# Kernel tuning notes

Measured on AMD Instinct MI355X. Metric: run time of the kernel, lower is better.

## Reference

```python
import jax, jax.numpy as jnp
import numpy as np

B, T, E, H = 4, 2048, 1024, 16
D = E // H
PAD_TOKEN_ID = 0
VOCAB = 50257


def setup_inputs() -> dict:
    key = jax.random.key(0)
    k1, k2, k3, k4 = jax.random.split(key, 4)
    x = jax.random.normal(k1, (B, T, E), dtype=jnp.float32)
    input_ids = jax.random.randint(k2, (B, T), 0, VOCAB, dtype=jnp.int64)
    # guarantee first key of every sequence is non-pad so no softmax row is fully masked
    input_ids = input_ids.at[:, 0].set(1)
    w_qkv = jax.random.normal(k3, (E, 3 * E), dtype=jnp.float32) * 0.02
    w_out = jax.random.normal(k4, (E, E), dtype=jnp.float32) * 0.02
    b_out = jnp.zeros((E,), dtype=jnp.float32)
    return {"x": x, "input_ids": input_ids, "w_qkv": w_qkv, "w_out": w_out, "b_out": b_out}


def reference(x, input_ids, w_qkv, w_out, b_out):
    b, t, e = x.shape
    # fused QKV projection (bias=False in original)
    qkv = x @ w_qkv                                   # [B,T,3E]
    q, k, v = jnp.split(qkv, 3, axis=-1)
    q = q.reshape(b, t, H, D).transpose(0, 2, 1, 3)   # [B,H,T,D]
    k = k.reshape(b, t, H, D).transpose(0, 2, 1, 3)
    v = v.reshape(b, t, H, D).transpose(0, 2, 1, 3)

    scale = 1.0 / jnp.sqrt(jnp.asarray(D, dtype=x.dtype))
    scores = jnp.einsum("bhqd,bhkd->bhqk", q, k) * scale   # [B,H,T,T]

    causal = jnp.tril(jnp.ones((t, t), dtype=bool))         # [T,T]
    key_keep = (input_ids != PAD_TOKEN_ID)[:, None, None, :]  # [B,1,1,T]
    mask = causal[None, None, :, :] & key_keep               # [B,1(T broadcast over H),T,T]
    scores = jnp.where(mask, scores, -jnp.inf)

    attn = jax.nn.softmax(scores, axis=-1)                   # dropout_p=0 in eval
    y = jnp.einsum("bhqk,bhkd->bhqd", attn, v)               # [B,H,T,D]
    y = y.transpose(0, 2, 1, 3).reshape(b, t, e)             # [B,T,E]
    return y @ w_out + b_out
```

## Files before the change

kernel.cpp:

```cpp
#include <hip/hip_runtime.h>
#include <hip/hip_bf16.h>
#include <stdint.h>

#define Hn 16
#define Tn 2048
#define En 1024
#define Dh 64

typedef __bf16 bf16x8 __attribute__((ext_vector_type(8)));
typedef float f32x4 __attribute__((ext_vector_type(4)));
typedef unsigned short u16;
typedef u16 u16x8 __attribute__((ext_vector_type(8)));

#define SCALE_Q 0.18033688f

__device__ __forceinline__ u16 f2bf(float f) {
  union { float f; uint32_t u; } v; v.f = f;
  uint32_t r = v.u + 0x7fffu + ((v.u >> 16) & 1u);
  return (u16)(r >> 16);
}

typedef const __attribute__((address_space(1))) void gvoid_t;
typedef __attribute__((address_space(3))) void lvoid_t;
__device__ __forceinline__ void gl_lds16(const void* g, void* l) {
  __builtin_amdgcn_global_load_lds((gvoid_t*)g, (lvoid_t*)l, 16, 0, 0);
}

__global__ void cvt_x_k(const float* __restrict__ in, u16* __restrict__ out) {
  int i = (blockIdx.x * 256 + threadIdx.x) * 8;
  float4 a = *(const float4*)(in + i);
  float4 b = *(const float4*)(in + i + 4);
  u16x8 o;
  o[0] = f2bf(a.x); o[1] = f2bf(a.y); o[2] = f2bf(a.z); o[3] = f2bf(a.w);
  o[4] = f2bf(b.x); o[5] = f2bf(b.y); o[6] = f2bf(b.z); o[7] = f2bf(b.w);
  *(u16x8*)(out + i) = o;
}

__global__ void transpose_cvt_k(const float* __restrict__ in, u16* __restrict__ out,
                                int R, int C) {
  __shared__ float tile[32][33];
  int c0 = blockIdx.x * 32, r0 = blockIdx.y * 32;
  for (int i = threadIdx.y; i < 32; i += 8)
    tile[i][threadIdx.x] = in[(size_t)(r0 + i) * C + c0 + threadIdx.x];
  __syncthreads();
  for (int i = threadIdx.y; i < 32; i += 8)
    out[(size_t)(c0 + i) * R + r0 + threadIdx.x] = f2bf(tile[threadIdx.x][i]);
}

__global__ void prep_mask_k(const int* __restrict__ in, float* __restrict__ maskf) {
  __shared__ int is64_s;
  if (threadIdx.x == 0) {
    int all0 = 1;
    for (int i = 1; i < 256; i += 2) all0 &= (in[i] == 0);
    is64_s = all0;
  }
  __syncthreads();
  int i = blockIdx.x * 256 + threadIdx.x;
  int v = is64_s ? in[2 * i] : in[i];
  maskf[i] = (v != 0) ? 0.f : -1e30f;
}

__device__ __forceinline__ void gemm_mainloop(const u16* __restrict__ A,
                                              const u16* __restrict__ Bt,
                                              int K, int m0, int n0,
                                              u16* lds, f32x4 acc[4][4]) {
  const int tid = threadIdx.x;
  const int lane = tid & 63;
  const int w = tid >> 6;
  const int wm = (w >> 1) * 64, wn = (w & 1) * 64;
  const int quad = lane >> 4, ln = lane & 15;

  const int e0 = w * 512 + lane * 8;
  const int r0 = e0 >> 5, c0 = e0 & 31;

  const u16* gA0 = A + (size_t)(m0 + r0) * K + c0;
  const u16* gA1 = gA0 + (size_t)64 * K;
  const u16* gB0 = Bt + (size_t)(n0 + r0) * K + c0;
  const u16* gB1 = gB0 + (size_t)64 * K;
  u16* lA0 = lds + e0;
  u16* lA1 = lds + e0 + 2048;
  u16* lB0 = lds + e0 + 4096;
  u16* lB1 = lds + e0 + 6144;

  for (int k0 = 0; k0 < K; k0 += 32) {
    gl_lds16(gA0 + k0, lA0);
    gl_lds16(gA1 + k0, lA1);
    gl_lds16(gB0 + k0, lB0);
    gl_lds16(gB1 + k0, lB1);
    __syncthreads();
    bf16x8 af[4], bfr[4];
#pragma unroll
    for (int mt = 0; mt < 4; mt++)
      af[mt] = *(const bf16x8*)(lds + (wm + mt * 16 + ln) * 32 + quad * 8);
#pragma unroll
    for (int nt = 0; nt < 4; nt++)
      bfr[nt] = *(const bf16x8*)(lds + 4096 + (wn + nt * 16 + ln) * 32 + quad * 8);
#pragma unroll
    for (int mt = 0; mt < 4; mt++)
#pragma unroll
      for (int nt = 0; nt < 4; nt++)
        acc[mt][nt] = __builtin_amdgcn_mfma_f32_16x16x32_bf16(af[mt], bfr[nt],
                                                              acc[mt][nt], 0, 0, 0);
    __syncthreads();
  }
}

__global__ __launch_bounds__(256, 3)
void gemm_qkv_kernel(const u16* __restrict__ X, const u16* __restrict__ Wt,
                     u16* __restrict__ Qo, u16* __restrict__ Ko,
                     u16* __restrict__ Vto) {
  __shared__ __align__(16) u16 lds[128 * 130];
  const int m0 = blockIdx.y * 128, n0 = blockIdx.x * 128;
  f32x4 acc[4][4];
#pragma unroll
  for (int i = 0; i < 4; i++)
#pragma unroll
    for (int j = 0; j < 4; j++) acc[i][j] = (f32x4){0.f, 0.f, 0.f, 0.f};

  gemm_mainloop(X, Wt, En, m0, n0, lds, acc);

  const int tid = threadIdx.x, lane = tid & 63, w = tid >> 6;
  const int wm = (w >> 1) * 64, wn = (w & 1) * 64;
  const int quad = lane >> 4, ln = lane & 15;
  const int which = n0 >> 10;
  const int bb = m0 >> 11, t0 = m0 & (Tn - 1);

  if (which < 2) {
#pragma unroll
    for (int mt = 0; mt < 4; mt++)
#pragma unroll
      for (int nt = 0; nt < 4; nt++)
#pragma unroll
        for (int r = 0; r < 4; r++) {
          int t = t0 + wm + mt * 16 + quad * 4 + r;
          int ng = n0 + wn + nt * 16 + ln;
          int e = ng & (En - 1);
          int h = e >> 6, d = e & 63;
          size_t bh = (size_t)(bb * Hn + h);
          if (which == 0)
            Qo[(bh * Tn + t) * Dh + d] = f2bf(acc[mt][nt][r] * SCALE_Q);
          else
            Ko[(bh * Tn + t) * Dh + d] = f2bf(acc[mt][nt][r]);
        }
  } else {
#pragma unroll
    for (int mt = 0; mt < 4; mt++)
#pragma unroll
      for (int nt = 0; nt < 4; nt++)
#pragma unroll
        for (int r = 0; r < 4; r++)
          lds[(wm + mt * 16 + quad * 4 + r) * 130 + wn + nt * 16 + ln] =
              f2bf(acc[mt][nt][r]);
    __syncthreads();
    const int ebase = n0 & (En - 1);
#pragma unroll
    for (int i = 0; i < 32; i++) {
      int col = w * 32 + i;
      int e = ebase + col;
      int hh = e >> 6, d = e & 63;
      size_t vrow = (((size_t)(bb * Hn + hh)) * Dh + d) * Tn + t0;
      Vto[vrow + lane] = lds[lane * 130 + col];
      Vto[vrow + 64 + lane] = lds[(64 + lane) * 130 + col];
    }
  }
}

__global__ __launch_bounds__(256, 3)
void gemm_out_kernel(const u16* __restrict__ Y, const u16* __restrict__ Wt,
                     const float* __restrict__ bias, float* __restrict__ Out) {
  __shared__ __align__(16) u16 lds[8192];
  const int m0 = blockIdx.y * 128, n0 = blockIdx.x * 128;
  f32x4 acc[4][4];
#pragma unroll
  for (int i = 0; i < 4; i++)
#pragma unroll
    for (int j = 0; j < 4; j++) acc[i][j] = (f32x4){0.f, 0.f, 0.f, 0.f};

  gemm_mainloop(Y, Wt, En, m0, n0, lds, acc);

  const int tid = threadIdx.x, lane = tid & 63, w = tid >> 6;
  const int wm = (w >> 1) * 64, wn = (w & 1) * 64;
  const int quad = lane >> 4, ln = lane & 15;

#pragma unroll
  for (int mt = 0; mt < 4; mt++)
#pragma unroll
    for (int nt = 0; nt < 4; nt++)
#pragma unroll
      for (int r = 0; r < 4; r++) {
        int mg = m0 + wm + mt * 16 + quad * 4 + r;
        int ng = n0 + wn + nt * 16 + ln;
        Out[(size_t)mg * En + ng] = acc[mt][nt][r] + bias[ng];
      }
}

__global__ __launch_bounds__(256, 3)
void attn_kernel(const u16* __restrict__ Q, const u16* __restrict__ K,
                 const u16* __restrict__ Vt, const float* __restrict__ maskf,
                 u16* __restrict__ Y) {
  __shared__ __align__(16) u16 Pl[128 * 76];
  __shared__ __align__(16) u16 KL[2 * 4096];

  const int bid = blockIdx.x;
  const int g = bid >> 8, sq = (bid >> 6) & 3;
  int qt;
  if (g == 0)      qt = 15 - sq;
  else if (g == 1) qt = sq;
  else if (g == 2) qt = 11 - sq;
  else             qt = 4 + sq;
  const int bh = bid & 63;
  const int b = bh >> 4, h = bh & 15;
  const int tid = threadIdx.x, lane = tid & 63, w = tid >> 6;
  const int quad = lane >> 4, ln = lane & 15;
  const int qb = w * 32;
  const int g0 = qt * 128 + qb;

  const size_t baseQK = (size_t)bh * (Tn * Dh);
  const size_t baseV = (size_t)bh * (Dh * Tn);
  const float* mrow = maskf + b * Tn;
  const u16* Kp = K + baseQK;

  const int srow = tid >> 3;
  const int scol = ((tid & 7) * 8) ^ ((srow & 7) * 8);
  const u16* gK0 = Kp + (size_t)srow * Dh + scol;
  const u16* gK1 = Kp + (size_t)(srow + 32) * Dh + scol;
  u16* lK0 = KL + tid * 8;
  u16* lK1 = lK0 + 2048;

  auto stage = [&](int buf, int k0) {
    gl_lds16(gK0 + (size_t)k0 * Dh, lK0 + buf * 4096);
    gl_lds16(gK1 + (size_t)k0 * Dh, lK1 + buf * 4096);
  };

  bf16x8 aq[2][2];
#pragma unroll
  for (int rt = 0; rt < 2; rt++)
#pragma unroll
    for (int ks = 0; ks < 2; ks++)
      aq[rt][ks] = *(const bf16x8*)(Q + baseQK +
          (size_t)(g0 + rt * 16 + ln) * Dh + ks * 32 + quad * 8);

  f32x4 O[2][4];
  float lsum[2][4];
#pragma unroll
  for (int rt = 0; rt < 2; rt++) {
#pragma unroll
    for (int dt = 0; dt < 4; dt++) O[rt][dt] = (f32x4){0.f, 0.f, 0.f, 0.f};
#pragma unroll
    for (int r = 0; r < 4; r++) lsum[rt][r] = 0.f;
  }

  auto tile = [&](const u16* kl, int k0, bool dg) {
    f32x4 s[2][4];
    {
      bf16x8 bk[4][2];
      float kvf[4];
#pragma unroll
      for (int ct = 0; ct < 4; ct++) {
        kvf[ct] = mrow[k0 + ct * 16 + ln];
#pragma unroll
        for (int ks = 0; ks < 2; ks++)
          bk[ct][ks] = *(const bf16x8*)(kl + (ct * 16 + ln) * 64 +
                                        ((ks * 32 + quad * 8) ^ ((ln & 7) * 8)));
      }
#pragma unroll
      for (int rt = 0; rt < 2; rt++)
#pragma unroll
        for (int ct = 0; ct < 4; ct++)
          s[rt][ct] = (f32x4){kvf[ct], kvf[ct], kvf[ct], kvf[ct]};
      __builtin_amdgcn_s_setprio(1);
#pragma unroll
      for (int ks = 0; ks < 2; ks++)
#pragma unroll
        for (int rt = 0; rt < 2; rt++)
#pragma unroll
          for (int ct = 0; ct < 4; ct++)
            s[rt][ct] = __builtin_amdgcn_mfma_f32_16x16x32_bf16(aq[rt][ks], bk[ct][ks],
                                                                s[rt][ct], 0, 0, 0);
      __builtin_amdgcn_s_setprio(0);
    }

    bf16x8 bv[4][2];
#pragma unroll
    for (int dt = 0; dt < 4; dt++)
#pragma unroll
      for (int ks = 0; ks < 2; ks++)
        bv[dt][ks] = *(const bf16x8*)(Vt + baseV +
            (size_t)(dt * 16 + ln) * Tn + k0 + ks * 32 + quad * 8);

#pragma unroll
    for (int rt = 0; rt < 2; rt++) {
      if (dg) {
#pragma unroll
        for (int ct = 0; ct < 4; ct++)
#pragma unroll
          for (int r = 0; r < 4; r++) {
            int qg = g0 + rt * 16 + quad * 4 + r;
            int kg = k0 + ct * 16 + ln;
            float v = (kg > qg) ? -1e30f : s[rt][ct][r];
            float p = exp2f(fminf(v, 126.f));
            lsum[rt][r] += p;
            Pl[(qb + rt * 16 + quad * 4 + r) * 76 + ct * 16 + ln] = f2bf(p);
          }
      } else {
#pragma unroll
        for (int ct = 0; ct < 4; ct++)
#pragma unroll
          for (int r = 0; r < 4; r++) {
            float p = exp2f(fminf(s[rt][ct][r], 126.f));
            lsum[rt][r] += p;
            Pl[(qb + rt * 16 + quad * 4 + r) * 76 + ct * 16 + ln] = f2bf(p);
          }
      }
    }

    __builtin_amdgcn_s_setprio(1);
#pragma unroll
    for (int ks2 = 0; ks2 < 2; ks2++)
#pragma unroll
      for (int rt = 0; rt < 2; rt++) {
        bf16x8 ap = *(const bf16x8*)(Pl + (qb + rt * 16 + ln) * 76 + ks2 * 32 + quad * 8);
#pragma unroll
        for (int dt = 0; dt < 4; dt++)
          O[rt][dt] = __builtin_amdgcn_mfma_f32_16x16x32_bf16(ap, bv[dt][ks2],
                                                              O[rt][dt], 0, 0, 0);
      }
    __builtin_amdgcn_s_setprio(0);
  };

  const int nfull = g0 >> 6;
  const int NT = 2 * qt + 1;
  stage(0, 0);
  int cur = 0;
  for (int kt = 0; kt <= NT; kt++) {
    __syncthreads();
    if (kt < NT) stage(cur ^ 1, (kt + 1) * 64);
    if (kt < nfull)       tile(KL + cur * 4096, kt * 64, false);
    else if (kt == nfull) tile(KL + cur * 4096, kt * 64, true);
    cur ^= 1;
  }

#pragma unroll
  for (int rt = 0; rt < 2; rt++)
#pragma unroll
    for (int r = 0; r < 4; r++) {
      float l = lsum[rt][r];
#pragma unroll
      for (int off = 1; off < 16; off <<= 1) l += __shfl_xor(l, off);
      float inv = 1.f / l;
      int tg = g0 + rt * 16 + quad * 4 + r;
      size_t ob = ((size_t)b * Tn + tg) * En + h * Dh;
#pragma unroll
      for (int dt = 0; dt < 4; dt++)
        Y[ob + dt * 16 + ln] = f2bf(O[rt][dt][r] * inv);
    }
}

#define OFF_MASK  0
#define OFF_WQKVT 16384
#define OFF_WOUTT (OFF_WQKVT + 3145728)
#define OFF_Q     (OFF_WOUTT + 1048576)
#define OFF_K     (OFF_Q + 8388608)
#define OFF_XY    (OFF_K + 8388608)

extern "C" void kernel_launch(void* const* d_in, const int* in_sizes, int n_in,
                              void* d_out, int out_size, void* d_ws, size_t ws_size,
                              hipStream_t stream) {
  const float* x = nullptr;
  const int* ids_raw = nullptr;
  const float* wqkv = nullptr;
  const float* wout = nullptr;
  const float* bias = nullptr;
  for (int i = 0; i < n_in; i++) {
    switch (in_sizes[i]) {
      case 8388608: x = (const float*)d_in[i]; break;
      case 8192:    ids_raw = (const int*)d_in[i]; break;
      case 3145728: wqkv = (const float*)d_in[i]; break;
      case 1048576: wout = (const float*)d_in[i]; break;
      case 1024:    bias = (const float*)d_in[i]; break;
      default: break;
    }
  }
  if (!x) x = (const float*)d_in[0];
  if (!ids_raw) ids_raw = (const int*)d_in[1];
  if (!wqkv) wqkv = (const float*)d_in[2];
  if (!wout) wout = (const float*)d_in[3];
  if (!bias) bias = (const float*)d_in[4];

  u16* ws = (u16*)d_ws;
  float* maskf = (float*)(ws + OFF_MASK);
  u16* wqkv_t = ws + OFF_WQKVT;
  u16* wout_t = ws + OFF_WOUTT;
  u16* Qb = ws + OFF_Q;
  u16* Kb = ws + OFF_K;
  u16* XbYb = ws + OFF_XY;
  u16* Vtb = (u16*)d_out;
  float* out = (float*)d_out;

  prep_mask_k<<<32, 256, 0, stream>>>(ids_raw, maskf);
  cvt_x_k<<<4096, 256, 0, stream>>>(x, XbYb);
  transpose_cvt_k<<<dim3(96, 32), dim3(32, 8), 0, stream>>>(wqkv, wqkv_t, 1024, 3072);
  transpose_cvt_k<<<dim3(32, 32), dim3(32, 8), 0, stream>>>(wout, wout_t, 1024, 1024);
  gemm_qkv_kernel<<<dim3(24, 64), 256, 0, stream>>>(XbYb, wqkv_t, Qb, Kb, Vtb);
  attn_kernel<<<1024, 256, 0, stream>>>(Qb, Kb, Vtb, maskf, XbYb);
  gemm_out_kernel<<<dim3(8, 64), 256, 0, stream>>>(XbYb, wout_t, bias, out);
}
```

Measured before the change: 288.3 us.

## Double GEMM k-tile depth to 64 with XOR-swizzled LDS layout

```diff
diff --git a/kernel.cpp b/kernel.cpp
--- a/kernel.cpp
+++ b/kernel.cpp
@@ -15,9 +15,8 @@
 #define SCALE_Q 0.18033688f
 
 __device__ __forceinline__ u16 f2bf(float f) {
-  union { float f; uint32_t u; } v; v.f = f;
-  uint32_t r = v.u + 0x7fffu + ((v.u >> 16) & 1u);
-  return (u16)(r >> 16);
+  __bf16 b = (__bf16)f;
+  return __builtin_bit_cast(u16, b);
 }
 
 typedef const __attribute__((address_space(1))) void gvoid_t;
@@ -71,36 +70,40 @@
   const int quad = lane >> 4, ln = lane & 15;
 
   const int e0 = w * 512 + lane * 8;
-  const int r0 = e0 >> 5, c0 = e0 & 31;
-
-  const u16* gA0 = A + (size_t)(m0 + r0) * K + c0;
-  const u16* gA1 = gA0 + (size_t)64 * K;
-  const u16* gB0 = Bt + (size_t)(n0 + r0) * K + c0;
-  const u16* gB1 = gB0 + (size_t)64 * K;
-  u16* lA0 = lds + e0;
-  u16* lA1 = lds + e0 + 2048;
-  u16* lB0 = lds + e0 + 4096;
-  u16* lB1 = lds + e0 + 6144;
-
-  for (int k0 = 0; k0 < K; k0 += 32) {
-    gl_lds16(gA0 + k0, lA0);
-    gl_lds16(gA1 + k0, lA1);
-    gl_lds16(gB0 + k0, lB0);
-    gl_lds16(gB1 + k0, lB1);
+  const int r0 = e0 >> 6;
+  const int cS = (e0 & 63) ^ ((r0 & 7) * 8);
+
+  const u16* gA = A + (size_t)(m0 + r0) * K + cS;
+  const u16* gB = Bt + (size_t)(n0 + r0) * K + cS;
+  u16* lA = lds + e0;
+  u16* lB = lds + 8192 + e0;
+  const int xA = (ln & 7) * 8;
+
+  for (int k0 = 0; k0 < K; k0 += 64) {
+#pragma unroll
+    for (int c = 0; c < 4; c++) {
+      gl_lds16(gA + (size_t)(c * 32) * K + k0, lA + c * 2048);
+      gl_lds16(gB + (size_t)(c * 32) * K + k0, lB + c * 2048);
+    }
     __syncthreads();
-    bf16x8 af[4], bfr[4];
-#pragma unroll
-    for (int mt = 0; mt < 4; mt++)
-      af[mt] = *(const bf16x8*)(lds + (wm + mt * 16 + ln) * 32 + quad * 8);
-#pragma unroll
-    for (int nt = 0; nt < 4; nt++)
-      bfr[nt] = *(const bf16x8*)(lds + 4096 + (wn + nt * 16 + ln) * 32 + quad * 8);
-#pragma unroll
-    for (int mt = 0; mt < 4; mt++)
+#pragma unroll
+    for (int kk = 0; kk < 2; kk++) {
+      bf16x8 af[4], bfr[4];
+#pragma unroll
+      for (int mt = 0; mt < 4; mt++)
+        af[mt] = *(const bf16x8*)(lds + (wm + mt * 16 + ln) * 64 +
+                                  ((kk * 32 + quad * 8) ^ xA));
 #pragma unroll
       for (int nt = 0; nt < 4; nt++)
-        acc[mt][nt] = __builtin_amdgcn_mfma_f32_16x16x32_bf16(af[mt], bfr[nt],
-                                                              acc[mt][nt], 0, 0, 0);
+        bfr[nt] = *(const bf16x8*)(lds + 8192 + (wn + nt * 16 + ln) * 64 +
+                                   ((kk * 32 + quad * 8) ^ xA));
+#pragma unroll
+      for (int mt = 0; mt < 4; mt++)
+#pragma unroll
+        for (int nt = 0; nt < 4; nt++)
+          acc[mt][nt] = __builtin_amdgcn_mfma_f32_16x16x32_bf16(af[mt], bfr[nt],
+                                                                acc[mt][nt], 0, 0, 0);
+    }
     __syncthreads();
   }
 }
@@ -168,7 +171,7 @@
 __global__ __launch_bounds__(256, 3)
 void gemm_out_kernel(const u16* __restrict__ Y, const u16* __restrict__ Wt,
                      const float* __restrict__ bias, float* __restrict__ Out) {
-  __shared__ __align__(16) u16 lds[8192];
+  __shared__ __align__(16) u16 lds[16384];
   const int m0 = blockIdx.y * 128, n0 = blockIdx.x * 128;
   f32x4 acc[4][4];
 #pragma unroll
```

Result: no change. 283.7 us (-1.6%).
